# Optimization experiments

Hardware: AMD Instinct MI355X
Metric: run time of the kernel (lower is better)

The kernel has to match this reference:

```python
import jax, jax.numpy as jnp
import numpy as np

EMBED_DIM = 1024
NUM_HEADS = 16
HEAD_DIM = EMBED_DIM // NUM_HEADS


def setup_inputs() -> dict:
    key = jax.random.key(0)
    k_x, k_qkv, k_w, k_b = jax.random.split(key, 4)
    B, N, C = 2, 2048, EMBED_DIM
    scale = 1.0 / np.sqrt(C)
    x = jax.random.normal(k_x, (B, N, C), dtype=jnp.float32)
    # nn.Linear(embed_dim, 3*embed_dim, bias=False): weight [3C, C]
    w_qkv = jax.random.normal(k_qkv, (3 * C, C), dtype=jnp.float32) * scale
    # nn.Linear(embed_dim, embed_dim): weight [C, C], bias [C]
    w_out = jax.random.normal(k_w, (C, C), dtype=jnp.float32) * scale
    b_out = jax.random.normal(k_b, (C,), dtype=jnp.float32) * scale
    return {"x": x, "w_qkv": w_qkv, "w_out": w_out, "b_out": b_out}


def reference(x, w_qkv, w_out, b_out):
    B, N, C = x.shape
    H, D = NUM_HEADS, HEAD_DIM
    # qkv projection: [B,N,3C] -> [3,B,H,N,D]
    qkv = jnp.einsum("bnc,fc->bnf", x, w_qkv)
    qkv = qkv.reshape(B, N, 3, H, D).transpose(2, 0, 3, 1, 4)
    q, k, v = qkv[0], qkv[1], qkv[2]
    # scaled dot-product attention (dropout p=0 / eval mode -> identity)
    scores = jnp.einsum("bhnd,bhmd->bhnm", q, k) / np.sqrt(D).astype(x.dtype)
    attn = jax.nn.softmax(scores, axis=-1)
    out = jnp.einsum("bhnm,bhmd->bhnd", attn, v)
    out = out.transpose(0, 2, 1, 3).reshape(B, N, C)
    return jnp.einsum("bnc,oc->bno", out, w_out) + b_out
```

## Files before the change

### kernel.cpp

```cpp
#include <hip/hip_runtime.h>
#include <hip/hip_bf16.h>

typedef unsigned short u16;
typedef __attribute__((ext_vector_type(4))) float f32x4;
typedef __attribute__((ext_vector_type(8))) short bf16x8;

#define MFMA16(a, b, c) __builtin_amdgcn_mfma_f32_16x16x32_bf16(a, b, c, 0, 0, 0)

__device__ __forceinline__ u16 f2bf(float f) {
    union { float f; unsigned u; } v;
    v.f = f;
    unsigned r = v.u + 0x7FFFu + ((v.u >> 16) & 1u);
    return (u16)(r >> 16);
}

__device__ __forceinline__ int4 pack8(const float4 a, const float4 b) {
    int4 r;
    r.x = (int)((unsigned)f2bf(a.x) | ((unsigned)f2bf(a.y) << 16));
    r.y = (int)((unsigned)f2bf(a.z) | ((unsigned)f2bf(a.w) << 16));
    r.z = (int)((unsigned)f2bf(b.x) | ((unsigned)f2bf(b.y) << 16));
    r.w = (int)((unsigned)f2bf(b.z) | ((unsigned)f2bf(b.w) << 16));
    return r;
}

__device__ __forceinline__ unsigned pk2(float a, float b) {
    __hip_bfloat162 t = __float22bfloat162_rn(make_float2(a, b));
    union { __hip_bfloat162 h; unsigned u; } c;
    c.h = t;
    return c.u;
}

__device__ __forceinline__ bf16x8 mk_pa(f32x4 a, f32x4 b) {
    union { uint4 u; bf16x8 v; } r;
    r.u.x = pk2(a[0], a[1]);
    r.u.y = pk2(a[2], a[3]);
    r.u.z = pk2(b[0], b[1]);
    r.u.w = pk2(b[2], b[3]);
    return r.v;
}

__device__ __forceinline__ void gload_lds16(const u16* g, u16* l) {
    __builtin_amdgcn_global_load_lds(
        (const __attribute__((address_space(1))) void*)g,
        (__attribute__((address_space(3))) void*)l, 16, 0, 0);
}

__global__ __launch_bounds__(256) void cvt_kernel(
    const float* __restrict__ x, const float* __restrict__ wq,
    const float* __restrict__ wo, u16* __restrict__ outb)
{
    size_t i = ((size_t)blockIdx.x * 256 + threadIdx.x) * 8;
    const float* src;
    size_t off;
    if (i < 4194304)      { src = x;  off = i; }
    else if (i < 7340032) { src = wq; off = i - 4194304; }
    else                  { src = wo; off = i - 7340032; }
    float4 a = *(const float4*)(src + off);
    float4 b = *(const float4*)(src + off + 4);
    *(int4*)(outb + i) = pack8(a, b);
}

__global__ __launch_bounds__(512) void qkv_gemm_kernel(
    const u16* __restrict__ X, const u16* __restrict__ W,
    u16* __restrict__ qws, u16* __restrict__ kws, u16* __restrict__ vws)
{
    __shared__ __align__(16) u16 Ash[256 * 64];
    __shared__ __align__(16) u16 Bsh[128 * 64];
    const int id = blockIdx.x;
    const int xcd = id & 7, slot = id >> 3;
    const int bm = (xcd >> 1) * 4 + (slot & 3);
    const int bn = (xcd & 1) * 12 + (slot >> 2);
    const int tid = threadIdx.x;
    const int lane = tid & 63, wid = tid >> 6;
    const int wm = wid >> 1, wn = wid & 1;
    const int g = lane >> 4, lq = lane & 15;

    f32x4 acc[4][4];
#pragma unroll
    for (int i = 0; i < 4; i++)
#pragma unroll
        for (int j = 0; j < 4; j++) acc[i][j] = (f32x4){0.f, 0.f, 0.f, 0.f};

    const int lrow = lane >> 3;
    const int lchunk = (lane & 7) ^ lrow;
    const u16* Ab = X + (size_t)(bm * 256 + lrow) * 1024 + lchunk * 8;
    const u16* Bb = W + (size_t)(bn * 128 + lrow) * 1024 + lchunk * 8;

    for (int kt = 0; kt < 16; ++kt) {
#pragma unroll
        for (int i = 0; i < 4; i++) {
            int sub = wid * 4 + i;
            gload_lds16(Ab + (size_t)sub * 8192 + kt * 64, &Ash[sub * 512]);
        }
#pragma unroll
        for (int i = 0; i < 2; i++) {
            int sub = wid * 2 + i;
            gload_lds16(Bb + (size_t)sub * 8192 + kt * 64, &Bsh[sub * 512]);
        }
        __syncthreads();
#pragma unroll
        for (int ka = 0; ka < 2; ka++) {
            bf16x8 af[4], bfr[4];
#pragma unroll
            for (int mt = 0; mt < 4; mt++) {
                int row = wm * 64 + mt * 16 + lq;
                af[mt] = *(const bf16x8*)&Ash[row * 64 + (((ka * 4 + g) ^ (row & 7)) << 3)];
            }
#pragma unroll
            for (int nt = 0; nt < 4; nt++) {
                int row = wn * 64 + nt * 16 + lq;
                bfr[nt] = *(const bf16x8*)&Bsh[row * 64 + (((ka * 4 + g) ^ (row & 7)) << 3)];
            }
#pragma unroll
            for (int mt = 0; mt < 4; mt++)
#pragma unroll
                for (int nt = 0; nt < 4; nt++)
                    acc[mt][nt] = MFMA16(af[mt], bfr[nt], acc[mt][nt]);
        }
        __syncthreads();
    }

#pragma unroll
    for (int mt = 0; mt < 4; mt++) {
#pragma unroll
        for (int nt = 0; nt < 4; nt++) {
            int f = bn * 128 + wn * 64 + nt * 16 + lq;
            int t = f >> 10, h = (f >> 6) & 15, d = f & 63;
            int mbase = bm * 256 + wm * 64 + mt * 16 + g * 4;
            int b = mbase >> 11, n0 = mbase & 2047;
            if (t == 0) {
#pragma unroll
                for (int r = 0; r < 4; r++)
                    qws[((size_t)(b * 16 + h) * 2048 + n0 + r) * 64 + d] =
                        f2bf(acc[mt][nt][r] * 0.18033688f);
            } else if (t == 1) {
#pragma unroll
                for (int r = 0; r < 4; r++)
                    kws[((size_t)(b * 16 + h) * 2048 + n0 + r) * 64 + d] =
                        f2bf(acc[mt][nt][r]);
            } else {
                ushort4 pk;
                pk.x = f2bf(acc[mt][nt][0]);
                pk.y = f2bf(acc[mt][nt][1]);
                pk.z = f2bf(acc[mt][nt][2]);
                pk.w = f2bf(acc[mt][nt][3]);
                *(ushort4*)&vws[((size_t)(b * 16 + h) * 64 + d) * 2048 + n0] = pk;
            }
        }
    }
}

__global__ __launch_bounds__(256, 2) void attn_kernel(
    const u16* __restrict__ qws, const u16* __restrict__ kws,
    const u16* __restrict__ vws, float* __restrict__ Opart,
    float* __restrict__ lpart)
{
    __shared__ __align__(16) u16 Ksh[2][64 * 64];
    __shared__ __align__(16) u16 Vsh[2][64 * 64];
    const int bh = blockIdx.x, qt = blockIdx.y, kvh = blockIdx.z;
    const int tid = threadIdx.x, wid = tid >> 6, lane = tid & 63;
    const int g = lane >> 4, lq = lane & 15;

    const u16* Qp = qws + ((size_t)bh * 2048 + qt * 256 + wid * 64) * 64;
    bf16x8 qf[4][2];
#pragma unroll
    for (int qa = 0; qa < 4; qa++) {
        qf[qa][0] = *(const bf16x8*)(Qp + (qa * 16 + lq) * 64 + g * 8);
        qf[qa][1] = *(const bf16x8*)(Qp + (qa * 16 + lq) * 64 + 32 + g * 8);
    }

    const int lr8 = lane >> 3;
    const int c0 = ((lane & 7) - lr8) & 7;
    const u16* Kb = kws + (size_t)bh * 2048 * 64;
    const u16* Vb = vws + (size_t)bh * 64 * 2048;

#define STAGE(TG, BUF)                                                        \
    {                                                                         \
        _Pragma("unroll")                                                     \
        for (int i = 0; i < 2; i++) {                                         \
            int sub = wid * 2 + i;                                            \
            int c = (c0 - 2 * sub) & 7;                                       \
            gload_lds16(Kb + (size_t)((TG) * 64 + sub * 8 + lr8) * 64 + c * 8,\
                        &Ksh[BUF][sub * 512]);                                \
            gload_lds16(Vb + (size_t)(sub * 8 + lr8) * 2048 + (TG) * 64 + c * 8,\
                        &Vsh[BUF][sub * 512]);                                \
        }                                                                     \
    }

    int koff[4][2];
#pragma unroll
    for (int j = 0; j < 4; j++) {
        int R = (j >> 1) * 32 + (lq >> 2) * 8 + (j & 1) * 4 + (lq & 3);
        koff[j][0] = R * 64 + (((g)     + (R & 7) + 2 * (R >> 3)) & 7) * 8;
        koff[j][1] = R * 64 + (((4 + g) + (R & 7) + 2 * (R >> 3)) & 7) * 8;
    }
    int voff[4][2];
#pragma unroll
    for (int dt = 0; dt < 4; dt++) {
        int vr = dt * 16 + lq;
        voff[dt][0] = vr * 64 + (((g)     + (vr & 7) + 2 * (vr >> 3)) & 7) * 8;
        voff[dt][1] = vr * 64 + (((4 + g) + (vr & 7) + 2 * (vr >> 3)) & 7) * 8;
    }

    bf16x8 onesB;
#pragma unroll
    for (int i = 0; i < 8; i++) onesB[i] = (short)0x3F80;

    f32x4 oacc[4][4];
#pragma unroll
    for (int qa = 0; qa < 4; qa++)
#pragma unroll
        for (int i = 0; i < 4; i++) oacc[qa][i] = (f32x4){0.f, 0.f, 0.f, 0.f};
    f32x4 lacc[4];
#pragma unroll
    for (int qa = 0; qa < 4; qa++) lacc[qa] = (f32x4){0.f, 0.f, 0.f, 0.f};

    const int tbase = kvh * 16;
    STAGE(tbase, 0);

    for (int t = 0; t < 16; ++t) {
        const int buf = t & 1;
        STAGE(tbase + ((t + 1) & 15), buf ^ 1);
        asm volatile("s_waitcnt vmcnt(4)" ::: "memory");
        __builtin_amdgcn_s_barrier();
        __builtin_amdgcn_sched_barrier(0);

        const u16* Kt = Ksh[buf];
        const u16* Vt = Vsh[buf];

        bf16x8 pa0[4], pa1[4];
        {
            f32x4 za[4], zb[4];
            bf16x8 k0 = *(const bf16x8*)&Kt[koff[0][0]];
            bf16x8 k1 = *(const bf16x8*)&Kt[koff[0][1]];
#pragma unroll
            for (int qa = 0; qa < 4; qa++) {
                f32x4 z = (f32x4){0.f, 0.f, 0.f, 0.f};
                z = MFMA16(k0, qf[qa][0], z);
                z = MFMA16(k1, qf[qa][1], z);
                za[qa] = z;
            }
            k0 = *(const bf16x8*)&Kt[koff[1][0]];
            k1 = *(const bf16x8*)&Kt[koff[1][1]];
#pragma unroll
            for (int qa = 0; qa < 4; qa++) {
                f32x4 z = (f32x4){0.f, 0.f, 0.f, 0.f};
                z = MFMA16(k0, qf[qa][0], z);
                z = MFMA16(k1, qf[qa][1], z);
                zb[qa] = z;
            }
#pragma unroll
            for (int qa = 0; qa < 4; qa++) {
#pragma unroll
                for (int r = 0; r < 4; r++) {
                    za[qa][r] = __builtin_amdgcn_exp2f(za[qa][r]);
                    zb[qa][r] = __builtin_amdgcn_exp2f(zb[qa][r]);
                }
                pa0[qa] = mk_pa(za[qa], zb[qa]);
            }
            k0 = *(const bf16x8*)&Kt[koff[2][0]];
            k1 = *(const bf16x8*)&Kt[koff[2][1]];
#pragma unroll
            for (int qa = 0; qa < 4; qa++) {
                f32x4 z = (f32x4){0.f, 0.f, 0.f, 0.f};
                z = MFMA16(k0, qf[qa][0], z);
                z = MFMA16(k1, qf[qa][1], z);
                za[qa] = z;
            }
            k0 = *(const bf16x8*)&Kt[koff[3][0]];
            k1 = *(const bf16x8*)&Kt[koff[3][1]];
#pragma unroll
            for (int qa = 0; qa < 4; qa++) {
                f32x4 z = (f32x4){0.f, 0.f, 0.f, 0.f};
                z = MFMA16(k0, qf[qa][0], z);
                z = MFMA16(k1, qf[qa][1], z);
                zb[qa] = z;
            }
#pragma unroll
            for (int qa = 0; qa < 4; qa++) {
#pragma unroll
                for (int r = 0; r < 4; r++) {
                    za[qa][r] = __builtin_amdgcn_exp2f(za[qa][r]);
                    zb[qa][r] = __builtin_amdgcn_exp2f(zb[qa][r]);
                }
                pa1[qa] = mk_pa(za[qa], zb[qa]);
            }
        }

        __builtin_amdgcn_s_setprio(1);
#pragma unroll
        for (int qa = 0; qa < 4; qa++) {
            lacc[qa] = MFMA16(pa0[qa], onesB, lacc[qa]);
            lacc[qa] = MFMA16(pa1[qa], onesB, lacc[qa]);
        }
#pragma unroll
        for (int dt = 0; dt < 4; dt++) {
            bf16x8 vb0 = *(const bf16x8*)&Vt[voff[dt][0]];
            bf16x8 vb1 = *(const bf16x8*)&Vt[voff[dt][1]];
#pragma unroll
            for (int qa = 0; qa < 4; qa++) {
                oacc[qa][dt] = MFMA16(pa0[qa], vb0, oacc[qa][dt]);
                oacc[qa][dt] = MFMA16(pa1[qa], vb1, oacc[qa][dt]);
            }
        }
        __builtin_amdgcn_s_setprio(0);
        __builtin_amdgcn_s_barrier();
    }
#undef STAGE

    const int nbase = qt * 256 + wid * 64;
#pragma unroll
    for (int qa = 0; qa < 4; qa++) {
#pragma unroll
        for (int dt = 0; dt < 4; dt++)
#pragma unroll
            for (int r = 0; r < 4; r++) {
                int n = nbase + qa * 16 + g * 4 + r;
                Opart[(size_t)kvh * 4194304 + ((size_t)bh * 2048 + n) * 64 + dt * 16 + lq] =
                    oacc[qa][dt][r];
            }
        if (lq == 0) {
#pragma unroll
            for (int r = 0; r < 4; r++)
                lpart[kvh * 65536 + bh * 2048 + nbase + qa * 16 + g * 4 + r] =
                    lacc[qa][r];
        }
    }
}

__global__ __launch_bounds__(256) void combine_kernel(
    const float* __restrict__ Opart, const float* __restrict__ lpart,
    u16* __restrict__ ows)
{
    int idx = blockIdx.x * 256 + threadIdx.x;
    int d4 = (idx & 15) * 4;
    int n  = (idx >> 4) & 2047;
    int bh = idx >> 15;
    size_t o = ((size_t)bh * 2048 + n) * 64 + d4;
    float4 a = *(const float4*)(Opart + o);
    float4 c = *(const float4*)(Opart + 4194304 + o);
    float rl = 1.0f / (lpart[bh * 2048 + n] + lpart[65536 + bh * 2048 + n]);
    ushort4 pk;
    pk.x = f2bf((a.x + c.x) * rl);
    pk.y = f2bf((a.y + c.y) * rl);
    pk.z = f2bf((a.z + c.z) * rl);
    pk.w = f2bf((a.w + c.w) * rl);
    int b = bh >> 4, h = bh & 15;
    *(ushort4*)&ows[((size_t)b * 2048 + n) * 1024 + h * 64 + d4] = pk;
}

__global__ __launch_bounds__(512) void out_gemm_kernel(
    const u16* __restrict__ A, const u16* __restrict__ W,
    const float* __restrict__ bias, float* __restrict__ Out)
{
    __shared__ __align__(16) u16 Ash[256 * 64];
    __shared__ __align__(16) u16 Bsh[128 * 64];
    const int id = blockIdx.x;
    const int xcd = id & 7, slot = id >> 3;
    const int bm = xcd * 2 + (slot & 1);
    const int bn = slot >> 1;
    const int tid = threadIdx.x;
    const int lane = tid & 63, wid = tid >> 6;
    const int wm = wid >> 1, wn = wid & 1;
    const int g = lane >> 4, lq = lane & 15;

    f32x4 acc[4][4];
#pragma unroll
    for (int i = 0; i < 4; i++)
#pragma unroll
        for (int j = 0; j < 4; j++) acc[i][j] = (f32x4){0.f, 0.f, 0.f, 0.f};

    const int lrow = lane >> 3;
    const int lchunk = (lane & 7) ^ lrow;
    const u16* Ab = A + (size_t)(bm * 256 + lrow) * 1024 + lchunk * 8;
    const u16* Bb = W + (size_t)(bn * 128 + lrow) * 1024 + lchunk * 8;

    for (int kt = 0; kt < 16; ++kt) {
#pragma unroll
        for (int i = 0; i < 4; i++) {
            int sub = wid * 4 + i;
            gload_lds16(Ab + (size_t)sub * 8192 + kt * 64, &Ash[sub * 512]);
        }
#pragma unroll
        for (int i = 0; i < 2; i++) {
            int sub = wid * 2 + i;
            gload_lds16(Bb + (size_t)sub * 8192 + kt * 64, &Bsh[sub * 512]);
        }
        __syncthreads();
#pragma unroll
        for (int ka = 0; ka < 2; ka++) {
            bf16x8 af[4], bfr[4];
#pragma unroll
            for (int mt = 0; mt < 4; mt++) {
                int row = wm * 64 + mt * 16 + lq;
                af[mt] = *(const bf16x8*)&Ash[row * 64 + (((ka * 4 + g) ^ (row & 7)) << 3)];
            }
#pragma unroll
            for (int nt = 0; nt < 4; nt++) {
                int row = wn * 64 + nt * 16 + lq;
                bfr[nt] = *(const bf16x8*)&Bsh[row * 64 + (((ka * 4 + g) ^ (row & 7)) << 3)];
            }
#pragma unroll
            for (int mt = 0; mt < 4; mt++)
#pragma unroll
                for (int nt = 0; nt < 4; nt++)
                    acc[mt][nt] = MFMA16(af[mt], bfr[nt], acc[mt][nt]);
        }
        __syncthreads();
    }

#pragma unroll
    for (int mt = 0; mt < 4; mt++) {
#pragma unroll
        for (int nt = 0; nt < 4; nt++) {
            int ncol = bn * 128 + wn * 64 + nt * 16 + lq;
            float bv = bias[ncol];
            int mbase = bm * 256 + wm * 64 + mt * 16 + g * 4;
#pragma unroll
            for (int r = 0; r < 4; r++)
                Out[(size_t)(mbase + r) * 1024 + ncol] = acc[mt][nt][r] + bv;
        }
    }
}

extern "C" void kernel_launch(void* const* d_in, const int* in_sizes, int n_in,
                              void* d_out, int out_size, void* d_ws, size_t ws_size,
                              hipStream_t stream) {
    const float* x     = (const float*)d_in[0];
    const float* w_qkv = (const float*)d_in[1];
    const float* w_out = (const float*)d_in[2];
    const float* b_out = (const float*)d_in[3];
    float* out = (float*)d_out;

    u16* xb  = (u16*)d_ws;
    u16* wqb = xb + 4194304;
    u16* wob = wqb + 3145728;
    u16* qws = wob + 1048576;
    u16* kws = qws + 4194304;
    u16* vws = kws + 4194304;
    u16* ows = vws + 4194304;
    float* Opart = (float*)(ows + 4194304);
    float* lpart = Opart + 8388608;

    cvt_kernel<<<4096, 256, 0, stream>>>(x, w_qkv, w_out, xb);
    qkv_gemm_kernel<<<384, 512, 0, stream>>>(xb, wqb, qws, kws, vws);
    attn_kernel<<<dim3(32, 8, 2), 256, 0, stream>>>(qws, kws, vws, Opart, lpart);
    combine_kernel<<<4096, 256, 0, stream>>>(Opart, lpart, ows);
    out_gemm_kernel<<<128, 512, 0, stream>>>(ows, wob, b_out, out);
}
```

Baseline: 116.5 us.

## Split attention KV into four chunks with bf16 partial outputs

Attention now splits the KV sequence into four chunks instead of two, doubling the grid to 1024 blocks and raising the occupancy hint to 4 blocks per SM. Partial outputs are stored as bf16 rather than fp32 to halve the partial-buffer traffic, and the combine kernel sums four partials. The pipeline now issues the next tile's load after the barrier with a full vmcnt(0) wait and drops the trailing barrier, which reduces overlap and could race on the buffer being overwritten. The bf16 partials also add rounding error before normalization.

```diff
diff --git a/kernel.cpp b/kernel.cpp
--- a/kernel.cpp
+++ b/kernel.cpp
@@ -12,6 +12,12 @@
     v.f = f;
     unsigned r = v.u + 0x7FFFu + ((v.u >> 16) & 1u);
     return (u16)(r >> 16);
+}
+
+__device__ __forceinline__ float bf2f(u16 h) {
+    union { unsigned u; float f; } v;
+    v.u = ((unsigned)h) << 16;
+    return v.f;
 }
 
 __device__ __forceinline__ int4 pack8(const float4 a, const float4 b) {
@@ -150,9 +156,9 @@
     }
 }
 
-__global__ __launch_bounds__(256, 2) void attn_kernel(
+__global__ __launch_bounds__(256, 4) void attn_kernel(
     const u16* __restrict__ qws, const u16* __restrict__ kws,
-    const u16* __restrict__ vws, float* __restrict__ Opart,
+    const u16* __restrict__ vws, u16* __restrict__ Opart,
     float* __restrict__ lpart)
 {
     __shared__ __align__(16) u16 Ksh[2][64 * 64];
@@ -215,15 +221,15 @@
 #pragma unroll
     for (int qa = 0; qa < 4; qa++) lacc[qa] = (f32x4){0.f, 0.f, 0.f, 0.f};
 
-    const int tbase = kvh * 16;
-    STAGE(tbase, 0);
-
-    for (int t = 0; t < 16; ++t) {
+    const int tbase = kvh * 8;
+    STAGE(tbase + 0, 0);
+
+    for (int t = 0; t < 8; ++t) {
         const int buf = t & 1;
-        STAGE(tbase + ((t + 1) & 15), buf ^ 1);
-        asm volatile("s_waitcnt vmcnt(4)" ::: "memory");
+        asm volatile("s_waitcnt vmcnt(0)" ::: "memory");
         __builtin_amdgcn_s_barrier();
         __builtin_amdgcn_sched_barrier(0);
+        if (t < 7) STAGE(tbase + t + 1, buf ^ 1);
 
         const u16* Kt = Ksh[buf];
         const u16* Vt = Vsh[buf];
@@ -304,7 +310,6 @@
             }
         }
         __builtin_amdgcn_s_setprio(0);
-        __builtin_amdgcn_s_barrier();
     }
 #undef STAGE
 
@@ -317,7 +322,7 @@
             for (int r = 0; r < 4; r++) {
                 int n = nbase + qa * 16 + g * 4 + r;
                 Opart[(size_t)kvh * 4194304 + ((size_t)bh * 2048 + n) * 64 + dt * 16 + lq] =
-                    oacc[qa][dt][r];
+                    f2bf(oacc[qa][dt][r]);
             }
         if (lq == 0) {
 #pragma unroll
@@ -329,7 +334,7 @@
 }
 
 __global__ __launch_bounds__(256) void combine_kernel(
-    const float* __restrict__ Opart, const float* __restrict__ lpart,
+    const u16* __restrict__ Opart, const float* __restrict__ lpart,
     u16* __restrict__ ows)
 {
     int idx = blockIdx.x * 256 + threadIdx.x;
@@ -337,14 +342,22 @@
     int n  = (idx >> 4) & 2047;
     int bh = idx >> 15;
     size_t o = ((size_t)bh * 2048 + n) * 64 + d4;
-    float4 a = *(const float4*)(Opart + o);
-    float4 c = *(const float4*)(Opart + 4194304 + o);
-    float rl = 1.0f / (lpart[bh * 2048 + n] + lpart[65536 + bh * 2048 + n]);
+    float s0 = 0.f, s1 = 0.f, s2 = 0.f, s3 = 0.f, l = 0.f;
+#pragma unroll
+    for (int s = 0; s < 4; s++) {
+        ushort4 p = *(const ushort4*)(Opart + (size_t)s * 4194304 + o);
+        s0 += bf2f(p.x);
+        s1 += bf2f(p.y);
+        s2 += bf2f(p.z);
+        s3 += bf2f(p.w);
+        l += lpart[s * 65536 + bh * 2048 + n];
+    }
+    float rl = 1.0f / l;
     ushort4 pk;
-    pk.x = f2bf((a.x + c.x) * rl);
-    pk.y = f2bf((a.y + c.y) * rl);
-    pk.z = f2bf((a.z + c.z) * rl);
-    pk.w = f2bf((a.w + c.w) * rl);
+    pk.x = f2bf(s0 * rl);
+    pk.y = f2bf(s1 * rl);
+    pk.z = f2bf(s2 * rl);
+    pk.w = f2bf(s3 * rl);
     int b = bh >> 4, h = bh & 15;
     *(ushort4*)&ows[((size_t)b * 2048 + n) * 1024 + h * 64 + d4] = pk;
 }
@@ -439,12 +452,12 @@
     u16* kws = qws + 4194304;
     u16* vws = kws + 4194304;
     u16* ows = vws + 4194304;
-    float* Opart = (float*)(ows + 4194304);
-    float* lpart = Opart + 8388608;
+    u16* Opart = ows + 4194304;
+    float* lpart = (float*)(Opart + 16777216);
 
     cvt_kernel<<<4096, 256, 0, stream>>>(x, w_qkv, w_out, xb);
     qkv_gemm_kernel<<<384, 512, 0, stream>>>(xb, wqb, qws, kws, vws);
-    attn_kernel<<<dim3(32, 8, 2), 256, 0, stream>>>(qws, kws, vws, Opart, lpart);
+    attn_kernel<<<dim3(32, 8, 4), 256, 0, stream>>>(qws, kws, vws, Opart, lpart);
     combine_kernel<<<4096, 256, 0, stream>>>(Opart, lpart, ows);
     out_gemm_kernel<<<128, 512, 0, stream>>>(ows, wob, b_out, out);
 }
```

Result: slower. 239.1 us (+105.2%).
